# Kernel optimization log

Measured on AMD Instinct MI355X. Metric: run time of the kernel, lower is better.

## Reference

```python
import jax, jax.numpy as jnp
import numpy as np

B, T, DIM = 4, 2048, 64
NUM_CODES = 512

def setup_inputs() -> dict:
    key = jax.random.key(0)
    k1, k2 = jax.random.split(key)
    inputs = jax.random.normal(k1, (B, T, DIM), dtype=jnp.float32)
    # original init: truncated_normal(mean=0.5, stddev=0) -> constant 0.5; use
    # a real random codebook so argmin is non-degenerate, matching trained state
    lookup_table = jax.random.normal(k2, (NUM_CODES, DIM), dtype=jnp.float32)
    return {"inputs": inputs, "lookup_table": lookup_table}

def reference(inputs, lookup_table):
    # z: [B, T, 1, dim]; table: [1, 1, K, dim] -> diff [B, T, K, dim]
    diff = inputs[..., None, :] - lookup_table[None, None, :, :]
    dist = jnp.linalg.norm(diff, axis=-1)          # [B, T, K]
    k = jnp.argmin(dist, axis=-1)                  # [B, T] int
    z_q = jnp.take(lookup_table, k, axis=0)        # [B, T, dim]
    return (k, z_q)
```

## Files before the change

### kernel.cpp

```cpp
#include <hip/hip_runtime.h>
#include <math.h>


#define NQ      8192
#define VDIM    64
#define NCODES  512
#define NSPLIT  16
#define CODES_PER_CHUNK (NCODES / NSPLIT)

__global__ __launch_bounds__(256) void vq_partial_kernel(
    const float* __restrict__ inp,
    const float* __restrict__ table,
    float* __restrict__ wnorm,
    int* __restrict__ widx)
{
    const int lane = threadIdx.x & 63;
    const int wave = threadIdx.x >> 6;
    const int bq   = blockIdx.x >> 2;
    const int bc   = blockIdx.x & 3;
    const int part = bc * 4 + wave;
    const int q    = bq * 64 + lane;

    int cbase = part * CODES_PER_CHUNK;
    cbase = __builtin_amdgcn_readfirstlane(cbase);

    float qv[VDIM];
    const float4* qp = reinterpret_cast<const float4*>(inp + (size_t)q * VDIM);
#pragma unroll
    for (int i = 0; i < 16; ++i) {
        float4 v = qp[i];
        qv[4*i+0] = v.x; qv[4*i+1] = v.y; qv[4*i+2] = v.z; qv[4*i+3] = v.w;
    }

    float best = INFINITY;
    int   bidx = 0;

    for (int c = 0; c < CODES_PER_CHUNK; ++c) {
        const float4* crow = reinterpret_cast<const float4*>(table + (size_t)(cbase + c) * VDIM);
        float acc[8];
#pragma unroll
        for (int j = 0; j < 8; ++j) acc[j] = 0.0f;
#pragma unroll
        for (int i = 0; i < 16; ++i) {
            float4 cv = crow[i];
            float d0 = qv[4*i+0] - cv.x;
            float d1 = qv[4*i+1] - cv.y;
            float d2 = qv[4*i+2] - cv.z;
            float d3 = qv[4*i+3] - cv.w;
            acc[(4*i+0) & 7] = __builtin_fmaf(d0, d0, acc[(4*i+0) & 7]);
            acc[(4*i+1) & 7] = __builtin_fmaf(d1, d1, acc[(4*i+1) & 7]);
            acc[(4*i+2) & 7] = __builtin_fmaf(d2, d2, acc[(4*i+2) & 7]);
            acc[(4*i+3) & 7] = __builtin_fmaf(d3, d3, acc[(4*i+3) & 7]);
        }
        float s = ((acc[0] + acc[1]) + (acc[2] + acc[3]))
                + ((acc[4] + acc[5]) + (acc[6] + acc[7]));
        float n = sqrtf(s);
        if (n < best) {
            best = n;
            bidx = cbase + c;
        }
    }

    wnorm[(size_t)part * NQ + q] = best;
    widx [(size_t)part * NQ + q] = bidx;
}

__global__ __launch_bounds__(256) void vq_finalize_kernel(
    const float* __restrict__ table,
    const float* __restrict__ wnorm,
    const int* __restrict__ widx,
    float* __restrict__ out)
{
    const int gid = blockIdx.x * 256 + threadIdx.x;
    const int q = gid >> 6;
    const int d = gid & 63;

    float best = INFINITY;
    int   bidx = 0;
#pragma unroll
    for (int p = 0; p < NSPLIT; ++p) {
        float n = wnorm[(size_t)p * NQ + q];
        int   i = widx [(size_t)p * NQ + q];
        if (n < best) { best = n; bidx = i; }
    }

    out[NQ + (size_t)q * VDIM + d] = table[(size_t)bidx * VDIM + d];
    if (d == 0) out[q] = (float)bidx;
}

extern "C" void kernel_launch(void* const* d_in, const int* in_sizes, int n_in,
                              void* d_out, int out_size, void* d_ws, size_t ws_size,
                              hipStream_t stream) {
    const float* inp   = (const float*)d_in[0];
    const float* table = (const float*)d_in[1];
    float* out = (float*)d_out;

    float* wnorm = (float*)d_ws;
    int*   widx  = (int*)(wnorm + (size_t)NSPLIT * NQ);

    vq_partial_kernel<<<dim3(128 * 4), dim3(256), 0, stream>>>(inp, table, wnorm, widx);

    vq_finalize_kernel<<<dim3((NQ * VDIM) / 256), dim3(256), 0, stream>>>(table, wnorm, widx, out);
}
```

Measured before the change: 34.02 us.

## Stage codebook chunk in LDS and split codes across more blocks

Each block now copies its chunk of codebook rows into shared memory once. All four waves then read the codes from LDS instead of from global memory through scalar/vector loads. The code split is raised to 32 chunks when the workspace allows, which doubles the partial-result traffic and the finalize loop length but exposes more blocks. The change adds launch_bounds occupancy hints and a loop unroll of 2, and the finalize kernel takes nsplit at runtime instead of as a compile-time constant.

```diff
diff --git a/kernel.cpp b/kernel.cpp
--- a/kernel.cpp
+++ b/kernel.cpp
@@ -5,38 +5,48 @@
 #define NQ      8192
 #define VDIM    64
 #define NCODES  512
-#define NSPLIT  16
-#define CODES_PER_CHUNK (NCODES / NSPLIT)
 
-__global__ __launch_bounds__(256) void vq_partial_kernel(
+template <int NSPLIT>
+__global__ __launch_bounds__(256, 4) void vq_partial_kernel(
     const float* __restrict__ inp,
     const float* __restrict__ table,
     float* __restrict__ wnorm,
     int* __restrict__ widx)
 {
-    const int lane = threadIdx.x & 63;
-    const int wave = threadIdx.x >> 6;
-    const int bq   = blockIdx.x >> 2;
-    const int bc   = blockIdx.x & 3;
-    const int part = bc * 4 + wave;
-    const int q    = bq * 64 + lane;
+    constexpr int CPC = NCODES / NSPLIT;
+    __shared__ float lcode[CPC * VDIM];
 
-    int cbase = part * CODES_PER_CHUNK;
-    cbase = __builtin_amdgcn_readfirstlane(cbase);
+    const int lane  = threadIdx.x & 63;
+    const int wave  = threadIdx.x >> 6;
+    const int chunk = blockIdx.x % NSPLIT;
+    const int qquad = blockIdx.x / NSPLIT;
+    const int q     = qquad * 256 + wave * 64 + lane;
+
+    {
+        const float4* src = reinterpret_cast<const float4*>(table + (size_t)chunk * CPC * VDIM);
+        float4* dst = reinterpret_cast<float4*>(lcode);
+        constexpr int NV4 = CPC * VDIM / 4;
+#pragma unroll
+        for (int i = threadIdx.x; i < NV4; i += 256) dst[i] = src[i];
+    }
+    __syncthreads();
 
     float qv[VDIM];
-    const float4* qp = reinterpret_cast<const float4*>(inp + (size_t)q * VDIM);
+    {
+        const float4* qp = reinterpret_cast<const float4*>(inp + (size_t)q * VDIM);
 #pragma unroll
-    for (int i = 0; i < 16; ++i) {
-        float4 v = qp[i];
-        qv[4*i+0] = v.x; qv[4*i+1] = v.y; qv[4*i+2] = v.z; qv[4*i+3] = v.w;
+        for (int i = 0; i < 16; ++i) {
+            float4 v = qp[i];
+            qv[4*i+0] = v.x; qv[4*i+1] = v.y; qv[4*i+2] = v.z; qv[4*i+3] = v.w;
+        }
     }
 
     float best = INFINITY;
     int   bidx = 0;
 
-    for (int c = 0; c < CODES_PER_CHUNK; ++c) {
-        const float4* crow = reinterpret_cast<const float4*>(table + (size_t)(cbase + c) * VDIM);
+#pragma unroll 2
+    for (int c = 0; c < CPC; ++c) {
+        const float4* crow = reinterpret_cast<const float4*>(&lcode[c * VDIM]);
         float acc[8];
 #pragma unroll
         for (int j = 0; j < 8; ++j) acc[j] = 0.0f;
@@ -57,19 +67,20 @@
         float n = sqrtf(s);
         if (n < best) {
             best = n;
-            bidx = cbase + c;
+            bidx = chunk * CPC + c;
         }
     }
 
-    wnorm[(size_t)part * NQ + q] = best;
-    widx [(size_t)part * NQ + q] = bidx;
+    wnorm[(size_t)chunk * NQ + q] = best;
+    widx [(size_t)chunk * NQ + q] = bidx;
 }
 
 __global__ __launch_bounds__(256) void vq_finalize_kernel(
     const float* __restrict__ table,
     const float* __restrict__ wnorm,
     const int* __restrict__ widx,
-    float* __restrict__ out)
+    float* __restrict__ out,
+    int nsplit)
 {
     const int gid = blockIdx.x * 256 + threadIdx.x;
     const int q = gid >> 6;
@@ -77,8 +88,7 @@
 
     float best = INFINITY;
     int   bidx = 0;
-#pragma unroll
-    for (int p = 0; p < NSPLIT; ++p) {
+    for (int p = 0; p < nsplit; ++p) {
         float n = wnorm[(size_t)p * NQ + q];
         int   i = widx [(size_t)p * NQ + q];
         if (n < best) { best = n; bidx = i; }
@@ -95,10 +105,17 @@
     const float* table = (const float*)d_in[1];
     float* out = (float*)d_out;
 
-    float* wnorm = (float*)d_ws;
-    int*   widx  = (int*)(wnorm + (size_t)NSPLIT * NQ);
-
-    vq_partial_kernel<<<dim3(128 * 4), dim3(256), 0, stream>>>(inp, table, wnorm, widx);
-
-    vq_finalize_kernel<<<dim3((NQ * VDIM) / 256), dim3(256), 0, stream>>>(table, wnorm, widx, out);
+    if (ws_size >= (size_t)32 * NQ * 8) {
+        const int NS = 32;
+        float* wnorm = (float*)d_ws;
+        int*   widx  = (int*)(wnorm + (size_t)NS * NQ);
+        vq_partial_kernel<32><<<dim3(32 * NS), dim3(256), 0, stream>>>(inp, table, wnorm, widx);
+        vq_finalize_kernel<<<dim3((NQ * VDIM) / 256), dim3(256), 0, stream>>>(table, wnorm, widx, out, NS);
+    } else {
+        const int NS = 16;
+        float* wnorm = (float*)d_ws;
+        int*   widx  = (int*)(wnorm + (size_t)NS * NQ);
+        vq_partial_kernel<16><<<dim3(32 * NS), dim3(256), 0, stream>>>(inp, table, wnorm, widx);
+        vq_finalize_kernel<<<dim3((NQ * VDIM) / 256), dim3(256), 0, stream>>>(table, wnorm, widx, out, NS);
+    }
 }
```

After: 38.23 us. +12.4%, slower.
